# Performance work log

Measured on AMD Instinct MI355X. Metric: run time of the kernel, lower is better.

The kernel has to match this reference:

```python
import jax, jax.numpy as jnp
import numpy as np

N_NODES = 100000
N_EDGES = 1600000
N_GRAPHS = 1000
H = 4

def _ln(x, g, b, eps=1e-5):
    m = x.mean(-1, keepdims=True)
    v = ((x - m) ** 2).mean(-1, keepdims=True)
    return (x - m) / jnp.sqrt(v + eps) * g + b

def _gat(x, src, dst, W, att_src, att_dst, bias, C):
    # PyG GATConv (self-loops already appended to src/dst): per-edge scores,
    # segment softmax over incoming edges of each dst node, scatter-add aggregation.
    N = x.shape[0]
    h = (x @ W.T).reshape(N, H, C)                      # [N,H,C]
    a_s = (h * att_src[None]).sum(-1)                   # [N,H]
    a_d = (h * att_dst[None]).sum(-1)                   # [N,H]
    e = jax.nn.leaky_relu(a_s[src] + a_d[dst], 0.2)     # [E,H]
    m = jax.ops.segment_max(e, dst, num_segments=N)
    w = jnp.exp(e - m[dst])
    denom = jax.ops.segment_sum(w, dst, num_segments=N)
    alpha = w / denom[dst]
    out = jax.ops.segment_sum(alpha[:, :, None] * h[src], dst, num_segments=N)
    return out.reshape(N, H * C) + bias

def _mha_len1(y, in_w, in_b, out_w, out_b, d):
    # seq_len==1 (x.unsqueeze(0)): softmax over a single key is identically 1,
    # so MHA(y,y,y) == out_proj(v_proj(y)). Exactly the original math.
    v = y @ in_w[2 * d:3 * d].T + in_b[2 * d:3 * d]
    return v @ out_w.T + out_b

def _forward(x, edge_index, batch, fc_feat_w, fc_feat_b,
             gat1_w, gat1_as, gat1_ad, gat1_b,
             gat2_w, gat2_as, gat2_ad, gat2_b,
             enc_in_w, enc_in_b, enc_out_w, enc_out_b,
             enc_f1_w, enc_f1_b, enc_f2_w, enc_f2_b,
             enc_ln1_g, enc_ln1_b, enc_ln2_g, enc_ln2_b,
             dec_sa_in_w, dec_sa_in_b, dec_sa_out_w, dec_sa_out_b,
             dec_ca_in_w, dec_ca_in_b, dec_ca_out_w, dec_ca_out_b,
             dec_f1_w, dec_f1_b, dec_f2_w, dec_f2_b,
             dec_ln1_g, dec_ln1_b, dec_ln2_g, dec_ln2_b, dec_ln3_g, dec_ln3_b,
             fc_w, fc_b):
    N = x.shape[0]
    d = 16 * H  # 64
    loop = jnp.arange(N, dtype=edge_index.dtype)
    src = jnp.concatenate([edge_index[0], loop])  # add_self_loops=True (PyG default)
    dst = jnp.concatenate([edge_index[1], loop])
    h = x @ fc_feat_w.T + fc_feat_b                     # feature_fc: [N,8]
    h = jax.nn.leaky_relu(_gat(h, src, dst, gat1_w, gat1_as, gat1_ad, gat1_b, 32), 0.01)
    h = jax.nn.leaky_relu(_gat(h, src, dst, gat2_w, gat2_as, gat2_ad, gat2_b, 16), 0.01)
    y = h  # [N,64]; transformer sees (L=1, B=N, E=64)
    for i in range(2):  # encoder layers
        a = _mha_len1(y, enc_in_w[i], enc_in_b[i], enc_out_w[i], enc_out_b[i], d)
        y = _ln(y + a, enc_ln1_g[i], enc_ln1_b[i])
        f = jax.nn.relu(y @ enc_f1_w[i].T + enc_f1_b[i]) @ enc_f2_w[i].T + enc_f2_b[i]
        y = _ln(y + f, enc_ln2_g[i], enc_ln2_b[i])
    for i in range(2):  # decoder layers (memory == tgt)
        a = _mha_len1(y, dec_sa_in_w[i], dec_sa_in_b[i], dec_sa_out_w[i], dec_sa_out_b[i], d)
        y = _ln(y + a, dec_ln1_g[i], dec_ln1_b[i])
        a = _mha_len1(y, dec_ca_in_w[i], dec_ca_in_b[i], dec_ca_out_w[i], dec_ca_out_b[i], d)
        y = _ln(y + a, dec_ln2_g[i], dec_ln2_b[i])
        f = jax.nn.relu(y @ dec_f1_w[i].T + dec_f1_b[i]) @ dec_f2_w[i].T + dec_f2_b[i]
        y = _ln(y + f, dec_ln3_g[i], dec_ln3_b[i])
    sums = jax.ops.segment_sum(y, batch, num_segments=N_GRAPHS)
    cnts = jax.ops.segment_sum(jnp.ones((N,), y.dtype), batch, num_segments=N_GRAPHS)
    pooled = sums / jnp.maximum(cnts, 1.0)[:, None]     # global_mean_pool
    return pooled @ fc_w.T + fc_b

def setup_inputs() -> dict:
    key = jax.random.key(0)
    ks = iter(jax.random.split(key, 64))
    p = lambda *s: jax.random.normal(next(ks), s, dtype=jnp.float32) * 0.1
    d = 64
    inp = {
        'x': jax.random.normal(next(ks), (N_NODES, 4), dtype=jnp.float32),
        'edge_index': jax.random.randint(next(ks), (2, N_EDGES), 0, N_NODES, dtype=jnp.int32),
        'batch': jnp.sort(jax.random.randint(next(ks), (N_NODES,), 0, N_GRAPHS, dtype=jnp.int32)),
        'fc_feat_w': p(8, 4), 'fc_feat_b': p(8),
        'gat1_w': p(128, 8), 'gat1_as': p(H, 32), 'gat1_ad': p(H, 32), 'gat1_b': p(128),
        'gat2_w': p(64, 128), 'gat2_as': p(H, 16), 'gat2_ad': p(H, 16), 'gat2_b': p(64),
        'enc_in_w': p(2, 3 * d, d), 'enc_in_b': p(2, 3 * d), 'enc_out_w': p(2, d, d), 'enc_out_b': p(2, d),
        'enc_f1_w': p(2, 256, d), 'enc_f1_b': p(2, 256), 'enc_f2_w': p(2, d, 256), 'enc_f2_b': p(2, d),
        'enc_ln1_g': jnp.ones((2, d)), 'enc_ln1_b': jnp.zeros((2, d)),
        'enc_ln2_g': jnp.ones((2, d)), 'enc_ln2_b': jnp.zeros((2, d)),
        'dec_sa_in_w': p(2, 3 * d, d), 'dec_sa_in_b': p(2, 3 * d), 'dec_sa_out_w': p(2, d, d), 'dec_sa_out_b': p(2, d),
        'dec_ca_in_w': p(2, 3 * d, d), 'dec_ca_in_b': p(2, 3 * d), 'dec_ca_out_w': p(2, d, d), 'dec_ca_out_b': p(2, d),
        'dec_f1_w': p(2, 256, d), 'dec_f1_b': p(2, 256), 'dec_f2_w': p(2, d, 256), 'dec_f2_b': p(2, d),
        'dec_ln1_g': jnp.ones((2, d)), 'dec_ln1_b': jnp.zeros((2, d)),
        'dec_ln2_g': jnp.ones((2, d)), 'dec_ln2_b': jnp.zeros((2, d)),
        'dec_ln3_g': jnp.ones((2, d)), 'dec_ln3_b': jnp.zeros((2, d)),
        'fc_w': p(33, d), 'fc_b': p(33),
    }
    return inp

def reference(x, edge_index, batch, fc_feat_w, fc_feat_b,
              gat1_w, gat1_as, gat1_ad, gat1_b,
              gat2_w, gat2_as, gat2_ad, gat2_b,
              enc_in_w, enc_in_b, enc_out_w, enc_out_b,
              enc_f1_w, enc_f1_b, enc_f2_w, enc_f2_b,
              enc_ln1_g, enc_ln1_b, enc_ln2_g, enc_ln2_b,
              dec_sa_in_w, dec_sa_in_b, dec_sa_out_w, dec_sa_out_b,
              dec_ca_in_w, dec_ca_in_b, dec_ca_out_w, dec_ca_out_b,
              dec_f1_w, dec_f1_b, dec_f2_w, dec_f2_b,
              dec_ln1_g, dec_ln1_b, dec_ln2_g, dec_ln2_b, dec_ln3_g, dec_ln3_b,
              fc_w, fc_b):
    return _forward(x, edge_index, batch, fc_feat_w, fc_feat_b,
                    gat1_w, gat1_as, gat1_ad, gat1_b,
                    gat2_w, gat2_as, gat2_ad, gat2_b,
                    enc_in_w, enc_in_b, enc_out_w, enc_out_b,
                    enc_f1_w, enc_f1_b, enc_f2_w, enc_f2_b,
                    enc_ln1_g, enc_ln1_b, enc_ln2_g, enc_ln2_b,
                    dec_sa_in_w, dec_sa_in_b, dec_sa_out_w, dec_sa_out_b,
                    dec_ca_in_w, dec_ca_in_b, dec_ca_out_w, dec_ca_out_b,
                    dec_f1_w, dec_f1_b, dec_f2_w, dec_f2_b,
                    dec_ln1_g, dec_ln1_b, dec_ln2_g, dec_ln2_b, dec_ln3_g, dec_ln3_b,
                    fc_w, fc_b)
```

## Files before the change

kernel.cpp:

```cpp
#include <hip/hip_runtime.h>

#define NN 100000
#define NE 1600000
#define NG 1000
#define ETOT (NE + NN)
#define NODES_PER_GRP 12500

typedef _Float16 f16x8 __attribute__((ext_vector_type(8)));
typedef _Float16 f16x4 __attribute__((ext_vector_type(4)));
typedef _Float16 f16x2 __attribute__((ext_vector_type(2)));
typedef float f32x16 __attribute__((ext_vector_type(16)));
#define XROW 72

__global__ void k_h1(const float* __restrict__ x, const float* __restrict__ ffw,
                     const float* __restrict__ ffb, const float* __restrict__ g1w,
                     const float* __restrict__ asw, const float* __restrict__ adw,
                     _Float16* __restrict__ h1p, float* __restrict__ asp,
                     float* __restrict__ ad_) {
    int tid = blockIdx.x * 256 + threadIdx.x;
    int n = __builtin_amdgcn_readfirstlane(tid >> 6);
    int jp = threadIdx.x & 63;
    float xv[4];
#pragma unroll
    for (int k = 0; k < 4; k++) xv[k] = x[n * 4 + k];
    float h0[8];
#pragma unroll
    for (int o = 0; o < 8; o++) {
        float a = ffb[o];
#pragma unroll
        for (int k = 0; k < 4; k++) a = fmaf(xv[k], ffw[o * 4 + k], a);
        h0[o] = a;
    }
    const float* w0 = g1w + jp * 8;
    const float* w1 = g1w + (jp + 64) * 8;
    float a0 = 0.f, a1 = 0.f;
#pragma unroll
    for (int k = 0; k < 8; k++) { a0 = fmaf(h0[k], w0[k], a0); a1 = fmaf(h0[k], w1[k], a1); }
    f16x2 r; r[0] = (_Float16)a0; r[1] = (_Float16)a1;
    *(f16x2*)(h1p + ((size_t)n * 64 + jp) * 2) = r;
    float p0 = a0 * asw[jp], p1 = a1 * asw[jp + 64];
    float d0 = a0 * adw[jp], d1 = a1 * adw[jp + 64];
#pragma unroll
    for (int m = 1; m <= 16; m <<= 1) {
        p0 += __shfl_xor(p0, m, 64); p1 += __shfl_xor(p1, m, 64);
        d0 += __shfl_xor(d0, m, 64); d1 += __shfl_xor(d1, m, 64);
    }
    if ((jp & 31) == 0) {
        int half = jp >> 5;
        *(float2*)(asp + n * 4 + half * 2) = make_float2(p0, p1);
        ad_[n * 4 + half] = d0;
        ad_[n * 4 + 2 + half] = d1;
    }
}

__global__ void k_att2(const _Float16* __restrict__ h2h, const float* __restrict__ asw,
                       const float* __restrict__ adw, float* __restrict__ as_,
                       float* __restrict__ ad_) {
    int tid = blockIdx.x * 256 + threadIdx.x;
    if (tid >= NN * 4) return;
    int n = tid >> 2, h = tid & 3;
    const _Float16* hp = h2h + (size_t)n * 64 + h * 16;
    const float* ws_ = asw + h * 16;
    const float* wd_ = adw + h * 16;
    float a = 0.f, d = 0.f;
#pragma unroll
    for (int c = 0; c < 16; c++) {
        float hv = (float)hp[c];
        a = fmaf(hv, ws_[c], a); d = fmaf(hv, wd_[c], d);
    }
    as_[tid] = a; ad_[tid] = d;
}

__global__ void k_count(const int* __restrict__ ei, int* __restrict__ deg) {
    int g = blockIdx.x & 7;
    int bi = blockIdx.x >> 3;
    int nb = gridDim.x >> 3;
    int lo = g * NODES_PER_GRP, hi = lo + NODES_PER_GRP;
    for (int e = bi * 256 + threadIdx.x; e < ETOT; e += nb * 256) {
        int dst = (e < NE) ? ei[NE + e] : (e - NE);
        if (dst >= lo && dst < hi) atomicAdd(&deg[dst], 1);
    }
}

__global__ void k_scan1(const int* __restrict__ deg, int* __restrict__ offs, int* __restrict__ bsum) {
    __shared__ int s[1024];
    int tid = threadIdx.x;
    int i = blockIdx.x * 1024 + tid;
    int v = (i < NN) ? deg[i] : 0;
    s[tid] = v;
    __syncthreads();
    for (int d = 1; d < 1024; d <<= 1) {
        int t = 0;
        if (tid >= d) t = s[tid - d];
        __syncthreads();
        if (tid >= d) s[tid] += t;
        __syncthreads();
    }
    if (i < NN) offs[i] = s[tid] - v;
    if (tid == 1023) bsum[blockIdx.x] = s[tid];
}

__global__ void k_scan2(int* __restrict__ bsum) {
    __shared__ int s[128];
    int tid = threadIdx.x;
    int v = (tid < 98) ? bsum[tid] : 0;
    s[tid] = v;
    __syncthreads();
    for (int d = 1; d < 128; d <<= 1) {
        int t = 0;
        if (tid >= d) t = s[tid - d];
        __syncthreads();
        if (tid >= d) s[tid] += t;
        __syncthreads();
    }
    bsum[tid] = s[tid] - v;
}

__global__ void k_scan3(int* __restrict__ offs, const int* __restrict__ bsum, int* __restrict__ cur) {
    int i = blockIdx.x * 1024 + threadIdx.x;
    if (i < NN) {
        int v = offs[i] + bsum[blockIdx.x];
        offs[i] = v; cur[i] = v;
    }
    if (i == 0) offs[NN] = ETOT;
}

__global__ void k_scatter(const int* __restrict__ ei, int* __restrict__ cur, int* __restrict__ srcs) {
    int g = blockIdx.x & 7;
    int bi = blockIdx.x >> 3;
    int nb = gridDim.x >> 3;
    int lo = g * NODES_PER_GRP, hi = lo + NODES_PER_GRP;
    for (int e = bi * 256 + threadIdx.x; e < ETOT; e += nb * 256) {
        int dst = (e < NE) ? ei[NE + e] : (e - NE);
        if (dst >= lo && dst < hi) {
            int src = (e < NE) ? ei[e] : dst;
            int p = atomicAdd(&cur[dst], 1);
            srcs[p] = src;
        }
    }
}

__global__ void k_gat1(const int* __restrict__ offs, const int* __restrict__ srcs,
                       const float* __restrict__ asp, const float* __restrict__ ad_,
                       const _Float16* __restrict__ h1p, const float* __restrict__ bias,
                       _Float16* __restrict__ g1h) {
    int wid = __builtin_amdgcn_readfirstlane((blockIdx.x * 256 + threadIdx.x) >> 6);
    int lane = threadIdx.x & 63;
    if (wid >= NN) return;
    int off = offs[wid];
    int deg = offs[wid + 1] - off;
    int hA = lane >> 5;
    float4 adv = *(const float4*)(ad_ + wid * 4);
    float adA = hA ? adv.y : adv.x;
    float adB = hA ? adv.w : adv.z;
    float ws0 = 0.f, ws1 = 0.f, ac0 = 0.f, ac1 = 0.f;
    float ws0b = 0.f, ws1b = 0.f, ac0b = 0.f, ac1b = 0.f;
    for (int base = 0; base < deg; base += 64) {
        int idx = off + base + lane; if (idx >= ETOT) idx = ETOT - 1;
        int sv = srcs[idx];
        int cnt = deg - base; if (cnt > 64) cnt = 64;
        int j = 0;
        for (; j + 2 <= cnt; j += 2) {
            int sa = __builtin_amdgcn_readlane(sv, j);
            int sb = __builtin_amdgcn_readlane(sv, j + 1);
            float4 aa = *(const float4*)(asp + sa * 4);
            float4 ab = *(const float4*)(asp + sb * 4);
            f16x2 hpa = *(const f16x2*)(h1p + (size_t)sa * 128 + lane * 2);
            f16x2 hpb = *(const f16x2*)(h1p + (size_t)sb * 128 + lane * 2);
            float e0 = (hA ? aa.z : aa.x) + adA; e0 = fmaxf(e0, 0.2f * e0);
            float e1 = (hA ? aa.w : aa.y) + adB; e1 = fmaxf(e1, 0.2f * e1);
            float w0 = __expf(e0), w1 = __expf(e1);
            ws0 += w0; ws1 += w1;
            ac0 = fmaf(w0, (float)hpa[0], ac0); ac1 = fmaf(w1, (float)hpa[1], ac1);
            float e0b = (hA ? ab.z : ab.x) + adA; e0b = fmaxf(e0b, 0.2f * e0b);
            float e1b = (hA ? ab.w : ab.y) + adB; e1b = fmaxf(e1b, 0.2f * e1b);
            float w0b = __expf(e0b), w1b = __expf(e1b);
            ws0b += w0b; ws1b += w1b;
            ac0b = fmaf(w0b, (float)hpb[0], ac0b); ac1b = fmaf(w1b, (float)hpb[1], ac1b);
        }
        if (j < cnt) {
            int sa = __builtin_amdgcn_readlane(sv, j);
            float4 aa = *(const float4*)(asp + sa * 4);
            f16x2 hpa = *(const f16x2*)(h1p + (size_t)sa * 128 + lane * 2);
            float e0 = (hA ? aa.z : aa.x) + adA; e0 = fmaxf(e0, 0.2f * e0);
            float e1 = (hA ? aa.w : aa.y) + adB; e1 = fmaxf(e1, 0.2f * e1);
            float w0 = __expf(e0), w1 = __expf(e1);
            ws0 += w0; ws1 += w1;
            ac0 = fmaf(w0, (float)hpa[0], ac0); ac1 = fmaf(w1, (float)hpa[1], ac1);
        }
    }
    ws0 += ws0b; ws1 += ws1b; ac0 += ac0b; ac1 += ac1b;
    float v0 = ac0 / ws0 + bias[lane];      v0 = fmaxf(v0, 0.01f * v0);
    float v1 = ac1 / ws1 + bias[lane + 64]; v1 = fmaxf(v1, 0.01f * v1);
    g1h[(size_t)wid * 128 + lane] = (_Float16)v0;
    g1h[(size_t)wid * 128 + lane + 64] = (_Float16)v1;
}

__global__ void k_gat2(const int* __restrict__ offs, const int* __restrict__ srcs,
                       const float* __restrict__ as_, const float* __restrict__ ad_,
                       const _Float16* __restrict__ h2h, const float* __restrict__ bias,
                       _Float16* __restrict__ g2h) {
    int wid = __builtin_amdgcn_readfirstlane((blockIdx.x * 256 + threadIdx.x) >> 6);
    int lane = threadIdx.x & 63;
    if (wid >= NN) return;
    int off = offs[wid];
    int deg = offs[wid + 1] - off;
    int hd = lane >> 4;
    float4 adv = *(const float4*)(ad_ + wid * 4);
    float t01 = (hd & 1) ? adv.y : adv.x;
    float t23 = (hd & 1) ? adv.w : adv.z;
    float adA = (hd & 2) ? t23 : t01;
    float ws = 0.f, ac = 0.f, wsb = 0.f, acb = 0.f;
    for (int base = 0; base < deg; base += 64) {
        int idx = off + base + lane; if (idx >= ETOT) idx = ETOT - 1;
        int sv = srcs[idx];
        int cnt = deg - base; if (cnt > 64) cnt = 64;
        int j = 0;
        for (; j + 2 <= cnt; j += 2) {
            int sa = __builtin_amdgcn_readlane(sv, j);
            int sb = __builtin_amdgcn_readlane(sv, j + 1);
            float4 av = *(const float4*)(as_ + sa * 4);
            float4 bv = *(const float4*)(as_ + sb * 4);
            float ha = (float)h2h[(size_t)sa * 64 + lane];
            float hb = (float)h2h[(size_t)sb * 64 + lane];
            float u01 = (hd & 1) ? av.y : av.x, u23 = (hd & 1) ? av.w : av.z;
            float ea = ((hd & 2) ? u23 : u01) + adA; ea = fmaxf(ea, 0.2f * ea);
            float v01 = (hd & 1) ? bv.y : bv.x, v23 = (hd & 1) ? bv.w : bv.z;
            float eb = ((hd & 2) ? v23 : v01) + adA; eb = fmaxf(eb, 0.2f * eb);
            float wa = __expf(ea), wb = __expf(eb);
            ws += wa; ac = fmaf(wa, ha, ac);
            wsb += wb; acb = fmaf(wb, hb, acb);
        }
        if (j < cnt) {
            int sa = __builtin_amdgcn_readlane(sv, j);
            float4 av = *(const float4*)(as_ + sa * 4);
            float u01 = (hd & 1) ? av.y : av.x, u23 = (hd & 1) ? av.w : av.z;
            float ea = ((hd & 2) ? u23 : u01) + adA; ea = fmaxf(ea, 0.2f * ea);
            float wa = __expf(ea);
            ws += wa; ac = fmaf(wa, (float)h2h[(size_t)sa * 64 + lane], ac);
        }
    }
    ws += wsb; ac += acb;
    float v = ac / ws + bias[lane]; v = fmaxf(v, 0.01f * v);
    g2h[(size_t)wid * 64 + lane] = (_Float16)v;
}

#define GROW 136
#define CROW 72
__global__ __launch_bounds__(256, 2) void k_h2m(const _Float16* __restrict__ g1h,
                                                const _Float16* __restrict__ apw2,
                                                _Float16* __restrict__ h2h) {
    __shared__ _Float16 ls[4 * 32 * GROW];
    const int t = threadIdx.x;
    const int w = t >> 6, l = t & 63;
    const int col = l & 31, hf = l >> 5;
    const int wv = blockIdx.x * 4 + w;
    const int nb = wv * 32;
    if (nb >= NN) return;
    _Float16* g16 = ls + w * (32 * GROW);
    const int r = l >> 1, hb = l & 1;
    {
        int nr = nb + r; if (nr >= NN) nr = NN - 1;
        const _Float16* src = g1h + (size_t)nr * 128 + hb * 64;
        _Float16* dst = g16 + r * GROW + hb * 64;
#pragma unroll
        for (int q = 0; q < 8; q++)
            *(f16x8*)(dst + q * 8) = *(const f16x8*)(src + q * 8);
    }
    f16x8 bf[8];
#pragma unroll
    for (int ks = 0; ks < 8; ks++)
        bf[ks] = *(const f16x8*)(g16 + col * GROW + ks * 16 + hf * 8);
    f32x16 acc0, acc1;
#pragma unroll
    for (int i = 0; i < 16; i++) { acc0[i] = 0.f; acc1[i] = 0.f; }
#pragma unroll
    for (int ks = 0; ks < 8; ks++) {
        f16x8 a0 = *(const f16x8*)(apw2 + ((0 * 8 + ks) * 64 + l) * 8);
        f16x8 a1 = *(const f16x8*)(apw2 + ((1 * 8 + ks) * 64 + l) * 8);
        acc0 = __builtin_amdgcn_mfma_f32_32x32x16_f16(a0, bf[ks], acc0, 0, 0, 0);
        acc1 = __builtin_amdgcn_mfma_f32_32x32x16_f16(a1, bf[ks], acc1, 0, 0, 0);
    }
    _Float16* c16 = g16;
#pragma unroll
    for (int rg = 0; rg < 4; rg++) {
        f16x4 h0, h1;
#pragma unroll
        for (int i = 0; i < 4; i++) { h0[i] = (_Float16)acc0[rg * 4 + i]; h1[i] = (_Float16)acc1[rg * 4 + i]; }
        *(f16x4*)(c16 + col * CROW + rg * 8 + hf * 4) = h0;
        *(f16x4*)(c16 + col * CROW + 32 + rg * 8 + hf * 4) = h1;
    }
    if (nb + r < NN) {
        _Float16* dst = h2h + (size_t)(nb + r) * 64 + hb * 32;
        const _Float16* srow = c16 + r * CROW + hb * 32;
#pragma unroll
        for (int q = 0; q < 4; q++)
            *(f16x8*)(dst + q * 8) = *(const f16x8*)(srow + q * 8);
    }
}

__global__ void k_fuse(const float* __restrict__ enc_in_w, const float* __restrict__ enc_in_b,
                       const float* __restrict__ enc_out_w, const float* __restrict__ enc_out_b,
                       const float* __restrict__ sa_in_w, const float* __restrict__ sa_in_b,
                       const float* __restrict__ sa_out_w, const float* __restrict__ sa_out_b,
                       const float* __restrict__ ca_in_w, const float* __restrict__ ca_in_b,
                       const float* __restrict__ ca_out_w, const float* __restrict__ ca_out_b,
                       _Float16* __restrict__ apk, float* __restrict__ fb) {
    int tid = blockIdx.x * 256 + threadIdx.x;
    int p = tid >> 12, r = tid & 4095, j = r >> 6, k = r & 63;
    int li = p & 1;
    const float *iw, *ib, *ow, *ob;
    if (p < 2)      { iw = enc_in_w + li * 12288; ib = enc_in_b + li * 192; ow = enc_out_w + li * 4096; ob = enc_out_b + li * 64; }
    else if (p < 4) { iw = sa_in_w + li * 12288;  ib = sa_in_b + li * 192;  ow = sa_out_w + li * 4096;  ob = sa_out_b + li * 64; }
    else            { iw = ca_in_w + li * 12288;  ib = ca_in_b + li * 192;  ow = ca_out_w + li * 4096;  ob = ca_out_b + li * 64; }
    float a = 0.f;
    for (int m = 0; m < 64; m++) a = fmaf(ow[j * 64 + m], iw[(128 + m) * 64 + k], a);
    int l = ((k >> 3) & 1) * 32 + (j & 31);
    apk[p * 4096 + (((j >> 5) * 4 + (k >> 4)) * 64 + l) * 8 + (k & 7)] = (_Float16)a;
    if (k == 0) {
        float fa = ob[j];
        for (int m = 0; m < 64; m++) fa = fmaf(ow[j * 64 + m], ib[128 + m], fa);
        fb[p * 64 + j] = fa;
    }
}

#define APK_F1 24576
#define APK_F2 90112
#define APK_TOT 155648
__global__ void k_apack(const float* __restrict__ ef1, const float* __restrict__ df1,
                        const float* __restrict__ ef2, const float* __restrict__ df2,
                        const float* __restrict__ g2w, _Float16* __restrict__ apk,
                        _Float16* __restrict__ apw2) {
    int tid = blockIdx.x * 256 + threadIdx.x;
    if (tid < 65536) {
        int pl = tid >> 14, idx = tid & 16383;
        int mt = idx >> 11, ks = (idx >> 9) & 3, l = (idx >> 3) & 63, d = idx & 7;
        int m = mt * 32 + (l & 31), k = ks * 16 + (l >> 5) * 8 + d;
        const float* f1 = (pl < 2) ? ef1 + pl * 16384 : df1 + (pl - 2) * 16384;
        apk[APK_F1 + pl * 16384 + idx] = (_Float16)f1[m * 64 + k];
    } else if (tid < 131072) {
        int r = tid - 65536;
        int pl = r >> 14, idx = r & 16383;
        int mt = idx >> 13, ks = (idx >> 9) & 15, l = (idx >> 3) & 63, d = idx & 7;
        int m = mt * 32 + (l & 31), k = ks * 16 + (l >> 5) * 8 + d;
        const float* f2 = (pl < 2) ? ef2 + pl * 16384 : df2 + (pl - 2) * 16384;
        apk[APK_F2 + pl * 16384 + idx] = (_Float16)f2[m * 256 + k];
    } else {
        int r = tid - 131072;
        int mtks = r >> 9, l = (r >> 3) & 63, d = r & 7;
        int mt = mtks >> 3, ks = mtks & 7;
        int m = mt * 32 + (l & 31), k = ks * 16 + (l >> 5) * 8 + d;
        apw2[r] = (_Float16)g2w[m * 128 + k];
    }
}

struct XQ {
    const _Float16* apk; const float* fb;
    const float* ef1b; const float* ef2b; const float* df1b; const float* df2b;
    const float* el1g; const float* el1b; const float* el2g; const float* el2b;
    const float* dl1g; const float* dl1b; const float* dl2g; const float* dl2b;
    const float* dl3g; const float* dl3b;
};

__device__ __forceinline__ void xstore(_Float16* xw, const float y[4][16], int col, int hf) {
#pragma unroll
    for (int nt = 0; nt < 2; nt++)
#pragma unroll
        for (int mt = 0; mt < 2; mt++)
#pragma unroll
            for (int rg = 0; rg < 4; rg++) {
                f16x4 h4;
#pragma unroll
                for (int i = 0; i < 4; i++) h4[i] = (_Float16)y[mt * 2 + nt][rg * 4 + i];
                *(f16x4*)(xw + (nt * 32 + col) * XROW + mt * 32 + rg * 8 + hf * 4) = h4;
            }
}

__device__ __forceinline__ void loadbf(const _Float16* xw, f16x8 bf[2][4], int col, int hf) {
#pragma unroll
    for (int nt = 0; nt < 2; nt++)
#pragma unroll
        for (int ks = 0; ks < 4; ks++)
            bf[nt][ks] = *(const f16x8*)(xw + (nt * 32 + col) * XROW + ks * 16 + hf * 8);
}

__device__ __forceinline__ void lnw(float y[4][16], const float* g, const float* b, int hf) {
#pragma unroll
    for (int nt = 0; nt < 2; nt++) {
        float s = 0.f, q = 0.f;
#pragma unroll
        for (int mt = 0; mt < 2; mt++)
#pragma unroll
            for (int r = 0; r < 16; r++) { float v = y[mt * 2 + nt][r]; s += v; q = fmaf(v, v, q); }
        s += __shfl_xor(s, 32, 64);
        q += __shfl_xor(q, 32, 64);
        float m = s * 0.015625f;
        float var = fmaf(q, 0.015625f, -m * m);
        float rs = rsqrtf(var + 1e-5f);
#pragma unroll
        for (int mt = 0; mt < 2; mt++)
#pragma unroll
            for (int rg = 0; rg < 4; rg++) {
                float4 g4 = *(const float4*)(g + mt * 32 + rg * 8 + hf * 4);
                float4 b4 = *(const float4*)(b + mt * 32 + rg * 8 + hf * 4);
                float* yp = &y[mt * 2 + nt][rg * 4];
                yp[0] = fmaf((yp[0] - m) * rs, g4.x, b4.x);
                yp[1] = fmaf((yp[1] - m) * rs, g4.y, b4.y);
                yp[2] = fmaf((yp[2] - m) * rs, g4.z, b4.z);
                yp[3] = fmaf((yp[3] - m) * rs, g4.w, b4.w);
            }
    }
}

__global__ __launch_bounds__(256, 2) void k_xform(const _Float16* __restrict__ yin,
                                                  float* __restrict__ yout, XQ P) {
    __shared__ _Float16 xs[4 * 64 * XROW];
    __shared__ _Float16 wb[8192];
    const int t = threadIdx.x;
    const int w = t >> 6, l = t & 63;
    const int col = l & 31, hf = l >> 5;
    _Float16* xw = xs + w * (64 * XROW);
    const int nb = blockIdx.x * 256 + w * 64;
    const int nn0 = nb + col, nn1 = nb + 32 + col;
    const int nc0 = nn0 < NN ? nn0 : NN - 1;
    const int nc1 = nn1 < NN ? nn1 : NN - 1;

    float y[4][16];
#pragma unroll
    for (int mt = 0; mt < 2; mt++)
#pragma unroll
        for (int nt = 0; nt < 2; nt++) {
            const _Float16* src = yin + (size_t)(nt ? nc1 : nc0) * 64 + mt * 32 + hf * 4;
#pragma unroll
            for (int rg = 0; rg < 4; rg++) {
                f16x4 v = *(const f16x4*)(src + rg * 8);
#pragma unroll
                for (int i = 0; i < 4; i++) y[mt * 2 + nt][rg * 4 + i] = (float)v[i];
            }
        }
    f16x8 bf[2][4];
    xstore(xw, y, col, hf);
    loadbf(xw, bf, col, hf);

#pragma unroll 1
    for (int layer = 0; layer < 4; layer++) {
        const bool enc = layer < 2;
        const int li = enc ? layer : layer - 2;
        const int nat = enc ? 1 : 2;
#pragma unroll 1
        for (int at = 0; at < nat; at++) {
            const int p = enc ? layer : (at == 0 ? 2 + li : 4 + li);
            const _Float16* apA = P.apk + p * 4096;
            __syncthreads();
#pragma unroll
            for (int i = 0; i < 2; i++)
                *(f16x8*)(wb + (t + i * 256) * 8) = *(const f16x8*)(apA + (t + i * 256) * 8);
            __syncthreads();
            const float* fbp = P.fb + p * 64;
            f32x16 acc[4];
#pragma unroll
            for (int mt = 0; mt < 2; mt++) {
                f32x16 a;
#pragma unroll
                for (int rg = 0; rg < 4; rg++) {
                    float4 b4 = *(const float4*)(fbp + mt * 32 + rg * 8 + hf * 4);
                    a[rg * 4 + 0] = b4.x; a[rg * 4 + 1] = b4.y; a[rg * 4 + 2] = b4.z; a[rg * 4 + 3] = b4.w;
                }
                acc[mt * 2 + 0] = a; acc[mt * 2 + 1] = a;
            }
#pragma unroll
            for (int mt = 0; mt < 2; mt++)
#pragma unroll
                for (int ks = 0; ks < 4; ks++) {
                    f16x8 af = *(const f16x8*)(wb + ((mt * 4 + ks) * 64 + l) * 8);
                    acc[mt * 2 + 0] = __builtin_amdgcn_mfma_f32_32x32x16_f16(af, bf[0][ks], acc[mt * 2 + 0], 0, 0, 0);
                    acc[mt * 2 + 1] = __builtin_amdgcn_mfma_f32_32x32x16_f16(af, bf[1][ks], acc[mt * 2 + 1], 0, 0, 0);
                }
#pragma unroll
            for (int ti = 0; ti < 4; ti++)
#pragma unroll
                for (int r = 0; r < 16; r++) y[ti][r] += acc[ti][r];
            const float *g, *b;
            if (enc)          { g = P.el1g + li * 64; b = P.el1b + li * 64; }
            else if (at == 0) { g = P.dl1g + li * 64; b = P.dl1b + li * 64; }
            else              { g = P.dl2g + li * 64; b = P.dl2b + li * 64; }
            lnw(y, g, b, hf);
            xstore(xw, y, col, hf);
            loadbf(xw, bf, col, hf);
        }
        const int pl = enc ? layer : 2 + li;
        const _Float16* apF1 = P.apk + APK_F1 + pl * 16384;
        const _Float16* apF2 = P.apk + APK_F2 + pl * 16384;
        const float* f1bp = (enc ? P.ef1b : P.df1b) + li * 256;
        const float* f2bp = (enc ? P.ef2b : P.df2b) + li * 64;
        f32x16 out[4];
#pragma unroll
        for (int mt = 0; mt < 2; mt++) {
            f32x16 a;
#pragma unroll
            for (int rg = 0; rg < 4; rg++) {
                float4 b4 = *(const float4*)(f2bp + mt * 32 + rg * 8 + hf * 4);
                a[rg * 4 + 0] = b4.x; a[rg * 4 + 1] = b4.y; a[rg * 4 + 2] = b4.z; a[rg * 4 + 3] = b4.w;
            }
            out[mt * 2 + 0] = a; out[mt * 2 + 1] = a;
        }
#pragma unroll 1
        for (int c = 0; c < 4; c++) {
            __syncthreads();
#pragma unroll
            for (int i = 0; i < 2; i++)
                *(f16x8*)(wb + (t + i * 256) * 8) = *(const f16x8*)(apF1 + c * 4096 + (t + i * 256) * 8);
            *(f16x8*)(wb + 4096 + t * 8) = *(const f16x8*)(apF2 + c * 2048 + t * 8);
            *(f16x8*)(wb + 6144 + t * 8) = *(const f16x8*)(apF2 + 8192 + c * 2048 + t * 8);
            __syncthreads();
            f32x16 ha[4];
#pragma unroll
            for (int hmt = 0; hmt < 2; hmt++) {
                f32x16 a;
#pragma unroll
                for (int rg = 0; rg < 4; rg++) {
                    float4 b4 = *(const float4*)(f1bp + c * 64 + hmt * 32 + rg * 8 + hf * 4);
                    a[rg * 4 + 0] = b4.x; a[rg * 4 + 1] = b4.y; a[rg * 4 + 2] = b4.z; a[rg * 4 + 3] = b4.w;
                }
                ha[hmt * 2 + 0] = a; ha[hmt * 2 + 1] = a;
            }
#pragma unroll
            for (int hmt = 0; hmt < 2; hmt++)
#pragma unroll
                for (int ks = 0; ks < 4; ks++) {
                    f16x8 af = *(const f16x8*)(wb + ((hmt * 4 + ks) * 64 + l) * 8);
                    ha[hmt * 2 + 0] = __builtin_amdgcn_mfma_f32_32x32x16_f16(af, bf[0][ks], ha[hmt * 2 + 0], 0, 0, 0);
                    ha[hmt * 2 + 1] = __builtin_amdgcn_mfma_f32_32x32x16_f16(af, bf[1][ks], ha[hmt * 2 + 1], 0, 0, 0);
                }
#pragma unroll
            for (int nt = 0; nt < 2; nt++)
#pragma unroll
                for (int hmt = 0; hmt < 2; hmt++)
#pragma unroll
                    for (int rg = 0; rg < 4; rg++) {
                        f16x4 h4;
#pragma unroll
                        for (int i = 0; i < 4; i++)
                            h4[i] = (_Float16)fmaxf(ha[hmt * 2 + nt][rg * 4 + i], 0.f);
                        *(f16x4*)(xw + (nt * 32 + col) * XROW + hmt * 32 + rg * 8 + hf * 4) = h4;
                    }
#pragma unroll
            for (int ksl = 0; ksl < 4; ksl++) {
                f16x8 hbf0 = *(const f16x8*)(xw + col * XROW + ksl * 16 + hf * 8);
                f16x8 hbf1 = *(const f16x8*)(xw + (32 + col) * XROW + ksl * 16 + hf * 8);
#pragma unroll
                for (int mt = 0; mt < 2; mt++) {
                    f16x8 af = *(const f16x8*)(wb + 4096 + mt * 2048 + (ksl * 64 + l) * 8);
                    out[mt * 2 + 0] = __builtin_amdgcn_mfma_f32_32x32x16_f16(af, hbf0, out[mt * 2 + 0], 0, 0, 0);
                    out[mt * 2 + 1] = __builtin_amdgcn_mfma_f32_32x32x16_f16(af, hbf1, out[mt * 2 + 1], 0, 0, 0);
                }
            }
        }
#pragma unroll
        for (int ti = 0; ti < 4; ti++)
#pragma unroll
            for (int r = 0; r < 16; r++) y[ti][r] += out[ti][r];
        const float* g2 = (enc ? P.el2g : P.dl3g) + li * 64;
        const float* b2 = (enc ? P.el2b : P.dl3b) + li * 64;
        lnw(y, g2, b2, hf);
        if (layer < 3) {
            xstore(xw, y, col, hf);
            loadbf(xw, bf, col, hf);
        }
    }
#pragma unroll
    for (int mt = 0; mt < 2; mt++)
#pragma unroll
        for (int nt = 0; nt < 2; nt++) {
            int n = nt ? nn1 : nn0;
            if (n < NN) {
                float* dst = yout + (size_t)n * 64 + mt * 32 + hf * 4;
#pragma unroll
                for (int rg = 0; rg < 4; rg++) {
                    const float* yp = &y[mt * 2 + nt][rg * 4];
                    *(float4*)(dst + rg * 8) = make_float4(yp[0], yp[1], yp[2], yp[3]);
                }
            }
        }
}

__global__ void k_pool(const float* __restrict__ y, const int* __restrict__ batch,
                       float* __restrict__ pooled) {
    int b = blockIdx.x;
    int t = threadIdx.x;
    int ch = t & 63, r = t >> 6;
    int lo = 0, hi = NN;
    while (lo < hi) { int mid = (lo + hi) >> 1; if (batch[mid] < b) lo = mid + 1; else hi = mid; }
    int st = lo;
    hi = NN;
    while (lo < hi) { int mid = (lo + hi) >> 1; if (batch[mid] < b + 1) lo = mid + 1; else hi = mid; }
    int en = lo;
    float s = 0.f;
    for (int i = st + r; i < en; i += 4) s += y[(size_t)i * 64 + ch];
    __shared__ float red[256];
    red[t] = s;
    __syncthreads();
    if (t < 64) {
        float tot = red[t] + red[t + 64] + red[t + 128] + red[t + 192];
        int cnt = en - st; if (cnt < 1) cnt = 1;
        pooled[b * 64 + t] = tot / (float)cnt;
    }
}

__global__ void k_fc(const float* __restrict__ pooled, const float* __restrict__ fcw,
                     const float* __restrict__ fcb, float* __restrict__ out) {
    int tid = blockIdx.x * 256 + threadIdx.x;
    if (tid >= NG * 33) return;
    int g = tid / 33, o = tid - g * 33;
    const float* p = pooled + g * 64;
    const float* w = fcw + o * 64;
    float a0 = 0.f, a1 = 0.f, a2 = 0.f, a3 = 0.f;
#pragma unroll
    for (int k = 0; k < 16; k++) {
        a0 = fmaf(p[4 * k], w[4 * k], a0);
        a1 = fmaf(p[4 * k + 1], w[4 * k + 1], a1);
        a2 = fmaf(p[4 * k + 2], w[4 * k + 2], a2);
        a3 = fmaf(p[4 * k + 3], w[4 * k + 3], a3);
    }
    out[tid] = fcb[o] + (a0 + a1) + (a2 + a3);
}

extern "C" void kernel_launch(void* const* d_in, const int* in_sizes, int n_in,
                              void* d_out, int out_size, void* d_ws, size_t ws_size,
                              hipStream_t stream) {
    (void)in_sizes; (void)n_in; (void)out_size; (void)ws_size;
    char* ws = (char*)d_ws;
    size_t o = 0;
    auto A = [&](size_t b) { size_t r = o; o += (b + 255) & ~(size_t)255; return r; };
    _Float16* h1p = (_Float16*)(ws + A((size_t)NN * 128 * 2));
    _Float16* h2h = (_Float16*)(ws + A((size_t)NN * 64 * 2));
    _Float16* g1h = (_Float16*)(ws + A((size_t)NN * 128 * 2));
    _Float16* g2h = (_Float16*)(ws + A((size_t)NN * 64 * 2));
    float* f_y   = (float*)(ws + A((size_t)NN * 64 * 4));
    float* f_asp = (float*)(ws + A((size_t)NN * 4 * 4));
    float* f_ad1 = (float*)(ws + A((size_t)NN * 4 * 4));
    float* f_as2 = (float*)(ws + A((size_t)NN * 4 * 4));
    float* f_ad2 = (float*)(ws + A((size_t)NN * 4 * 4));
    int* i_off   = (int*)(ws + A((size_t)(NN + 1) * 4));
    int* i_cur   = (int*)(ws + A((size_t)NN * 4));
    int* i_deg   = (int*)(ws + A((size_t)NN * 4));
    int* i_bsum  = (int*)(ws + A((size_t)1024 * 4));
    int* i_srcs  = (int*)(ws + A((size_t)ETOT * 4));
    float* f_fb  = (float*)(ws + A((size_t)6 * 64 * 4));
    _Float16* f_apk = (_Float16*)(ws + A((size_t)APK_TOT * 2));
    _Float16* apw2  = (_Float16*)(ws + A((size_t)8192 * 2));
    float* f_pool= (float*)(ws + A((size_t)NG * 64 * 4));

    const float* x   = (const float*)d_in[0];
    const int* ei    = (const int*)d_in[1];
    const int* batch = (const int*)d_in[2];
    #define F32(i) ((const float*)d_in[i])

    hipMemsetAsync(i_deg, 0, (size_t)NN * 4, stream);
    k_h1<<<NN * 64 / 256, 256, 0, stream>>>(x, F32(3), F32(4), F32(5), F32(6), F32(7),
                                            h1p, f_asp, f_ad1);
    k_count<<<8 * 128, 256, 0, stream>>>(ei, i_deg);
    k_scan1<<<98, 1024, 0, stream>>>(i_deg, i_off, i_bsum);
    k_scan2<<<1, 128, 0, stream>>>(i_bsum);
    k_scan3<<<98, 1024, 0, stream>>>(i_off, i_bsum, i_cur);
    k_scatter<<<8 * 128, 256, 0, stream>>>(ei, i_cur, i_srcs);
    k_gat1<<<NN * 64 / 256, 256, 0, stream>>>(i_off, i_srcs, f_asp, f_ad1, h1p, F32(8), g1h);
    k_apack<<<544, 256, 0, stream>>>(F32(17), F32(33), F32(19), F32(35), F32(9), f_apk, apw2);
    k_h2m<<<(NN / 32 + 3) / 4, 256, 0, stream>>>(g1h, apw2, h2h);
    k_att2<<<(NN * 4 + 255) / 256, 256, 0, stream>>>(h2h, F32(10), F32(11), f_as2, f_ad2);
    k_gat2<<<NN * 64 / 256, 256, 0, stream>>>(i_off, i_srcs, f_as2, f_ad2, h2h, F32(12), g2h);
    k_fuse<<<24576 / 256, 256, 0, stream>>>(F32(13), F32(14), F32(15), F32(16),
                                            F32(25), F32(26), F32(27), F32(28),
                                            F32(29), F32(30), F32(31), F32(32),
                                            f_apk, f_fb);
    XQ Q;
    Q.apk = f_apk; Q.fb = f_fb;
    Q.ef1b = F32(18); Q.ef2b = F32(20);
    Q.df1b = F32(34); Q.df2b = F32(36);
    Q.el1g = F32(21); Q.el1b = F32(22); Q.el2g = F32(23); Q.el2b = F32(24);
    Q.dl1g = F32(37); Q.dl1b = F32(38); Q.dl2g = F32(39); Q.dl2b = F32(40);
    Q.dl3g = F32(41); Q.dl3b = F32(42);
    k_xform<<<(NN + 255) / 256, 256, 0, stream>>>(g2h, f_y, Q);
    k_pool<<<NG, 256, 0, stream>>>(f_y, batch, f_pool);
    k_fc<<<(NG * 33 + 255) / 256, 256, 0, stream>>>(f_pool, F32(43), F32(44), (float*)d_out);
    #undef F32
}
```

Baseline: 605.3 us.

## Precompute per-edge attention weights in separate edge-parallel kernels

Adds edge-parallel kernels that compute the leaky-relu and exp attention weights once per edge, stored as packed fp16, using a new per-edge dst array written by the scatter kernel. The GAT aggregation kernels then read these weights instead of gathering source attention scores and evaluating exp redundantly in every lane. This removes duplicated transcendental work and scattered float4 loads from the per-node loops. In exchange it adds two extra kernel launches, writes and reads an 8-byte-per-edge buffer plus a dst array, and rounds the weights to fp16.

```diff
diff --git a/kernel.cpp b/kernel.cpp
--- a/kernel.cpp
+++ b/kernel.cpp
@@ -125,7 +125,8 @@
     if (i == 0) offs[NN] = ETOT;
 }
 
-__global__ void k_scatter(const int* __restrict__ ei, int* __restrict__ cur, int* __restrict__ srcs) {
+__global__ void k_scatter(const int* __restrict__ ei, int* __restrict__ cur,
+                          int* __restrict__ srcs, int* __restrict__ dsts) {
     int g = blockIdx.x & 7;
     int bi = blockIdx.x >> 3;
     int nb = gridDim.x >> 3;
@@ -136,23 +137,58 @@
             int src = (e < NE) ? ei[e] : dst;
             int p = atomicAdd(&cur[dst], 1);
             srcs[p] = src;
-        }
-    }
+            dsts[p] = dst;
+        }
+    }
+}
+
+__global__ void k_ew1(const int* __restrict__ srcs, const int* __restrict__ dsts,
+                      const float* __restrict__ asp, const float* __restrict__ ad_,
+                      uint2* __restrict__ ew) {
+    int p = blockIdx.x * 256 + threadIdx.x;
+    if (p >= ETOT) return;
+    int s = srcs[p], d = dsts[p];
+    float4 a = *(const float4*)(asp + s * 4);
+    float4 b = *(const float4*)(ad_ + d * 4);
+    float e0 = a.x + b.x; e0 = fmaxf(e0, 0.2f * e0);
+    float e2 = a.y + b.z; e2 = fmaxf(e2, 0.2f * e2);
+    float e1 = a.z + b.y; e1 = fmaxf(e1, 0.2f * e1);
+    float e3 = a.w + b.w; e3 = fmaxf(e3, 0.2f * e3);
+    union { unsigned u; _Float16 h[2]; } c0, c1;
+    c0.h[0] = (_Float16)__expf(e0); c0.h[1] = (_Float16)__expf(e2);
+    c1.h[0] = (_Float16)__expf(e1); c1.h[1] = (_Float16)__expf(e3);
+    uint2 o; o.x = c0.u; o.y = c1.u;
+    ew[p] = o;
+}
+
+__global__ void k_ew2(const int* __restrict__ srcs, const int* __restrict__ dsts,
+                      const float* __restrict__ as_, const float* __restrict__ ad_,
+                      uint2* __restrict__ ew) {
+    int p = blockIdx.x * 256 + threadIdx.x;
+    if (p >= ETOT) return;
+    int s = srcs[p], d = dsts[p];
+    float4 a = *(const float4*)(as_ + s * 4);
+    float4 b = *(const float4*)(ad_ + d * 4);
+    float e0 = a.x + b.x; e0 = fmaxf(e0, 0.2f * e0);
+    float e1 = a.y + b.y; e1 = fmaxf(e1, 0.2f * e1);
+    float e2 = a.z + b.z; e2 = fmaxf(e2, 0.2f * e2);
+    float e3 = a.w + b.w; e3 = fmaxf(e3, 0.2f * e3);
+    union { unsigned u; _Float16 h[2]; } c0, c1;
+    c0.h[0] = (_Float16)__expf(e0); c0.h[1] = (_Float16)__expf(e1);
+    c1.h[0] = (_Float16)__expf(e2); c1.h[1] = (_Float16)__expf(e3);
+    uint2 o; o.x = c0.u; o.y = c1.u;
+    ew[p] = o;
 }
 
 __global__ void k_gat1(const int* __restrict__ offs, const int* __restrict__ srcs,
-                       const float* __restrict__ asp, const float* __restrict__ ad_,
-                       const _Float16* __restrict__ h1p, const float* __restrict__ bias,
-                       _Float16* __restrict__ g1h) {
+                       const uint2* __restrict__ ew, const _Float16* __restrict__ h1p,
+                       const float* __restrict__ bias, _Float16* __restrict__ g1h) {
     int wid = __builtin_amdgcn_readfirstlane((blockIdx.x * 256 + threadIdx.x) >> 6);
     int lane = threadIdx.x & 63;
     if (wid >= NN) return;
     int off = offs[wid];
     int deg = offs[wid + 1] - off;
     int hA = lane >> 5;
-    float4 adv = *(const float4*)(ad_ + wid * 4);
-    float adA = hA ? adv.y : adv.x;
-    float adB = hA ? adv.w : adv.z;
     float ws0 = 0.f, ws1 = 0.f, ac0 = 0.f, ac1 = 0.f;
     float ws0b = 0.f, ws1b = 0.f, ac0b = 0.f, ac1b = 0.f;
     for (int base = 0; base < deg; base += 64) {
@@ -163,28 +199,27 @@
         for (; j + 2 <= cnt; j += 2) {
             int sa = __builtin_amdgcn_readlane(sv, j);
             int sb = __builtin_amdgcn_readlane(sv, j + 1);
-            float4 aa = *(const float4*)(asp + sa * 4);
-            float4 ab = *(const float4*)(asp + sb * 4);
+            uint2 wva = ew[off + base + j];
+            uint2 wvb = ew[off + base + j + 1];
             f16x2 hpa = *(const f16x2*)(h1p + (size_t)sa * 128 + lane * 2);
             f16x2 hpb = *(const f16x2*)(h1p + (size_t)sb * 128 + lane * 2);
-            float e0 = (hA ? aa.z : aa.x) + adA; e0 = fmaxf(e0, 0.2f * e0);
-            float e1 = (hA ? aa.w : aa.y) + adB; e1 = fmaxf(e1, 0.2f * e1);
-            float w0 = __expf(e0), w1 = __expf(e1);
+            union { unsigned u; _Float16 h[2]; } ca, cb;
+            ca.u = hA ? wva.y : wva.x;
+            cb.u = hA ? wvb.y : wvb.x;
+            float w0 = (float)ca.h[0], w1 = (float)ca.h[1];
+            float w0b = (float)cb.h[0], w1b = (float)cb.h[1];
             ws0 += w0; ws1 += w1;
             ac0 = fmaf(w0, (float)hpa[0], ac0); ac1 = fmaf(w1, (float)hpa[1], ac1);
-            float e0b = (hA ? ab.z : ab.x) + adA; e0b = fmaxf(e0b, 0.2f * e0b);
-            float e1b = (hA ? ab.w : ab.y) + adB; e1b = fmaxf(e1b, 0.2f * e1b);
-            float w0b = __expf(e0b), w1b = __expf(e1b);
             ws0b += w0b; ws1b += w1b;
             ac0b = fmaf(w0b, (float)hpb[0], ac0b); ac1b = fmaf(w1b, (float)hpb[1], ac1b);
         }
         if (j < cnt) {
             int sa = __builtin_amdgcn_readlane(sv, j);
-            float4 aa = *(const float4*)(asp + sa * 4);
+            uint2 wva = ew[off + base + j];
             f16x2 hpa = *(const f16x2*)(h1p + (size_t)sa * 128 + lane * 2);
-            float e0 = (hA ? aa.z : aa.x) + adA; e0 = fmaxf(e0, 0.2f * e0);
-            float e1 = (hA ? aa.w : aa.y) + adB; e1 = fmaxf(e1, 0.2f * e1);
-            float w0 = __expf(e0), w1 = __expf(e1);
+            union { unsigned u; _Float16 h[2]; } ca;
+            ca.u = hA ? wva.y : wva.x;
+            float w0 = (float)ca.h[0], w1 = (float)ca.h[1];
             ws0 += w0; ws1 += w1;
             ac0 = fmaf(w0, (float)hpa[0], ac0); ac1 = fmaf(w1, (float)hpa[1], ac1);
         }
@@ -197,19 +232,14 @@
 }
 
 __global__ void k_gat2(const int* __restrict__ offs, const int* __restrict__ srcs,
-                       const float* __restrict__ as_, const float* __restrict__ ad_,
-                       const _Float16* __restrict__ h2h, const float* __restrict__ bias,
-                       _Float16* __restrict__ g2h) {
+                       const uint2* __restrict__ ew, const _Float16* __restrict__ h2h,
+                       const float* __restrict__ bias, _Float16* __restrict__ g2h) {
     int wid = __builtin_amdgcn_readfirstlane((blockIdx.x * 256 + threadIdx.x) >> 6);
     int lane = threadIdx.x & 63;
     if (wid >= NN) return;
     int off = offs[wid];
     int deg = offs[wid + 1] - off;
     int hd = lane >> 4;
-    float4 adv = *(const float4*)(ad_ + wid * 4);
-    float t01 = (hd & 1) ? adv.y : adv.x;
-    float t23 = (hd & 1) ? adv.w : adv.z;
-    float adA = (hd & 2) ? t23 : t01;
     float ws = 0.f, ac = 0.f, wsb = 0.f, acb = 0.f;
     for (int base = 0; base < deg; base += 64) {
         int idx = off + base + lane; if (idx >= ETOT) idx = ETOT - 1;
@@ -219,24 +249,26 @@
         for (; j + 2 <= cnt; j += 2) {
             int sa = __builtin_amdgcn_readlane(sv, j);
             int sb = __builtin_amdgcn_readlane(sv, j + 1);
-            float4 av = *(const float4*)(as_ + sa * 4);
-            float4 bv = *(const float4*)(as_ + sb * 4);
+            uint2 wva = ew[off + base + j];
+            uint2 wvb = ew[off + base + j + 1];
             float ha = (float)h2h[(size_t)sa * 64 + lane];
             float hb = (float)h2h[(size_t)sb * 64 + lane];
-            float u01 = (hd & 1) ? av.y : av.x, u23 = (hd & 1) ? av.w : av.z;
-            float ea = ((hd & 2) ? u23 : u01) + adA; ea = fmaxf(ea, 0.2f * ea);
-            float v01 = (hd & 1) ? bv.y : bv.x, v23 = (hd & 1) ? bv.w : bv.z;
-            float eb = ((hd & 2) ? v23 : v01) + adA; eb = fmaxf(eb, 0.2f * eb);
-            float wa = __expf(ea), wb = __expf(eb);
+            unsigned sela = (hd & 2) ? wva.y : wva.x;
+            unsigned selb = (hd & 2) ? wvb.y : wvb.x;
+            union { unsigned u; _Float16 h[2]; } ca, cb;
+            ca.u = (hd & 1) ? (sela >> 16) : sela;
+            cb.u = (hd & 1) ? (selb >> 16) : selb;
+            float wa = (float)ca.h[0], wb = (float)cb.h[0];
             ws += wa; ac = fmaf(wa, ha, ac);
             wsb += wb; acb = fmaf(wb, hb, acb);
         }
         if (j < cnt) {
             int sa = __builtin_amdgcn_readlane(sv, j);
-            float4 av = *(const float4*)(as_ + sa * 4);
-            float u01 = (hd & 1) ? av.y : av.x, u23 = (hd & 1) ? av.w : av.z;
-            float ea = ((hd & 2) ? u23 : u01) + adA; ea = fmaxf(ea, 0.2f * ea);
-            float wa = __expf(ea);
+            uint2 wva = ew[off + base + j];
+            unsigned sela = (hd & 2) ? wva.y : wva.x;
+            union { unsigned u; _Float16 h[2]; } ca;
+            ca.u = (hd & 1) ? (sela >> 16) : sela;
+            float wa = (float)ca.h[0];
             ws += wa; ac = fmaf(wa, (float)h2h[(size_t)sa * 64 + lane], ac);
         }
     }
@@ -646,6 +678,8 @@
     int* i_deg   = (int*)(ws + A((size_t)NN * 4));
     int* i_bsum  = (int*)(ws + A((size_t)1024 * 4));
     int* i_srcs  = (int*)(ws + A((size_t)ETOT * 4));
+    int* i_dsts  = (int*)(ws + A((size_t)ETOT * 4));
+    uint2* e_w   = (uint2*)(ws + A((size_t)ETOT * 8));
     float* f_fb  = (float*)(ws + A((size_t)6 * 64 * 4));
     _Float16* f_apk = (_Float16*)(ws + A((size_t)APK_TOT * 2));
     _Float16* apw2  = (_Float16*)(ws + A((size_t)8192 * 2));
@@ -663,12 +697,14 @@
     k_scan1<<<98, 1024, 0, stream>>>(i_deg, i_off, i_bsum);
     k_scan2<<<1, 128, 0, stream>>>(i_bsum);
     k_scan3<<<98, 1024, 0, stream>>>(i_off, i_bsum, i_cur);
-    k_scatter<<<8 * 128, 256, 0, stream>>>(ei, i_cur, i_srcs);
-    k_gat1<<<NN * 64 / 256, 256, 0, stream>>>(i_off, i_srcs, f_asp, f_ad1, h1p, F32(8), g1h);
+    k_scatter<<<8 * 128, 256, 0, stream>>>(ei, i_cur, i_srcs, i_dsts);
+    k_ew1<<<(ETOT + 255) / 256, 256, 0, stream>>>(i_srcs, i_dsts, f_asp, f_ad1, e_w);
+    k_gat1<<<NN * 64 / 256, 256, 0, stream>>>(i_off, i_srcs, e_w, h1p, F32(8), g1h);
     k_apack<<<544, 256, 0, stream>>>(F32(17), F32(33), F32(19), F32(35), F32(9), f_apk, apw2);
     k_h2m<<<(NN / 32 + 3) / 4, 256, 0, stream>>>(g1h, apw2, h2h);
     k_att2<<<(NN * 4 + 255) / 256, 256, 0, stream>>>(h2h, F32(10), F32(11), f_as2, f_ad2);
-    k_gat2<<<NN * 64 / 256, 256, 0, stream>>>(i_off, i_srcs, f_as2, f_ad2, h2h, F32(12), g2h);
+    k_ew2<<<(ETOT + 255) / 256, 256, 0, stream>>>(i_srcs, i_dsts, f_as2, f_ad2, e_w);
+    k_gat2<<<NN * 64 / 256, 256, 0, stream>>>(i_off, i_srcs, e_w, h2h, F32(12), g2h);
     k_fuse<<<24576 / 256, 256, 0, stream>>>(F32(13), F32(14), F32(15), F32(16),
                                             F32(25), F32(26), F32(27), F32(28),
                                             F32(29), F32(30), F32(31), F32(32),
```

Measured after the change: 602.3 us (median of 2 runs). Within noise of the previous version (-0.5%).
